# Kernel tuning notes

Hardware: AMD Instinct MI355X
Metric: run time of the kernel (lower is better)

Reference implementation:

```python
import jax, jax.numpy as jnp
import numpy as np

N_HEADS = 16

def setup_inputs() -> dict:
    key = jax.random.key(0)
    ks = jax.random.split(key, 6)
    B, S, D = 2, 2048, 1024
    sc = 0.02
    return {
        "x": jax.random.normal(ks[0], (B, S, D), dtype=jnp.float32),
        "Wq": jax.random.normal(ks[1], (D, D), dtype=jnp.float32) * sc,
        "Wk": jax.random.normal(ks[2], (D, D), dtype=jnp.float32) * sc,
        "Wv": jax.random.normal(ks[3], (D, D), dtype=jnp.float32) * sc,
        "Wo": jax.random.normal(ks[4], (D, D), dtype=jnp.float32) * sc,
        "bo": jnp.zeros((D,), dtype=jnp.float32),
        "stride": 64,
    }

def _strided_mask(S: int, stride: int):
    # local window |i-j|<=1  OR  |i-j| == k*stride (k>=1); diff==0 is in the window
    i = jnp.arange(S)[:, None]
    j = jnp.arange(S)[None, :]
    diff = jnp.abs(i - j)
    return (diff <= 1) | (diff % stride == 0)  # [S, S] bool

def reference(x, Wq, Wk, Wv, Wo, bo, stride):
    B, S, D = x.shape
    H = N_HEADS
    Dh = D // H
    # q/k/v projections: nn.Linear(bias=False) applies x @ W.T
    def proj(W):
        return (x @ W.T).reshape(B, S, H, Dh).transpose(0, 2, 1, 3)  # [B,H,S,Dh]
    q, k, v = proj(Wq), proj(Wk), proj(Wv)
    scores = jnp.einsum('bhqd,bhkd->bhqk', q, k) / jnp.sqrt(jnp.float32(Dh))
    mask = _strided_mask(S, stride)  # [S,S]
    scores = jnp.where(mask[None, None], scores, -jnp.inf)
    attn = jax.nn.softmax(scores, axis=-1)  # dropout is identity in eval
    out = jnp.einsum('bhqk,bhkd->bhqd', attn, v)  # [B,H,S,Dh]
    out = out.transpose(0, 2, 1, 3).reshape(B, S, D)
    return out @ Wo.T + bo
```

## Files before the change

kernel.cpp:

```cpp
#include <hip/hip_runtime.h>
#include <hip/hip_bf16.h>


typedef __bf16 bf16;
typedef __attribute__((ext_vector_type(4))) __bf16 bf16x4;
typedef __attribute__((ext_vector_type(8))) __bf16 bf16x8;
typedef __attribute__((ext_vector_type(4))) float f32x4;
typedef __attribute__((ext_vector_type(4))) unsigned int u32x4;

constexpr int S_ = 2048;
constexpr int D_ = 1024;
constexpr int H_ = 16;
constexpr int DH = 64;
constexpr int M_ = 2 * S_;

__device__ __forceinline__ void gload_lds16(const bf16* g, bf16* l) {
    __builtin_amdgcn_global_load_lds(
        (const __attribute__((address_space(1))) void*)g,
        (__attribute__((address_space(3))) void*)l, 16, 0, 0);
}

#define BARRIER_FULL() do { asm volatile("" ::: "memory"); \
    __builtin_amdgcn_sched_barrier(0); \
    __builtin_amdgcn_s_barrier(); \
    __builtin_amdgcn_sched_barrier(0); \
    asm volatile("" ::: "memory"); } while (0)

#define WAIT_VM0() do { asm volatile("s_waitcnt vmcnt(0)" ::: "memory"); \
    __builtin_amdgcn_sched_barrier(0); } while (0)

#define WAIT_VM4() do { asm volatile("s_waitcnt vmcnt(4)" ::: "memory"); \
    __builtin_amdgcn_sched_barrier(0); } while (0)

__device__ __forceinline__ void stage32(const bf16* __restrict__ G, int base_row,
                                        int kcol, bf16* lds, int wave, int lane)
{
    const int rIn = lane >> 2;
    const int g   = (lane & 3) ^ ((lane >> 2) & 3) ^ (lane >> 4);
    #pragma unroll
    for (int l = 0; l < 2; ++l) {
        const int R = (wave * 2 + l) * 16;
        gload_lds16(G + (size_t)(base_row + R + rIn) * D_ + kcol + g * 8,
                    lds + R * 32);
    }
}

__global__ __launch_bounds__(512, 2)
void gemm_qkv_p2(const bf16* __restrict__ A,
                 const bf16* __restrict__ W,
                 bf16* __restrict__ C)
{
    constexpr int BK = 32;
    constexpr int NT = D_ / BK;
    constexpr int TSLOT = 256 * BK;
    __shared__ __align__(16) bf16 As[3 * TSLOT];
    __shared__ __align__(16) bf16 Bs[3 * TSLOT];

    const int tid  = threadIdx.x;
    const int wave = tid >> 6;
    const int lane = tid & 63;
    const int wm = wave >> 2;
    const int wn = wave & 3;

    const int lid = blockIdx.y * 12 + blockIdx.x;
    const int xcd = lid & 7, pos = lid >> 3;
    const int bxs = (xcd & 1) * 6 + pos % 6;
    const int bys = (xcd >> 1) * 4 + pos / 6;
    const int bm = bys * 256;
    const int bn = bxs * 256;

    const int l15 = lane & 15;
    const int rs  = (lane >> 4) ^ (lane & 3) ^ ((lane >> 2) & 3);
    const int aRd = wm * 4096 + l15 * 32 + rs * 8;
    const int bRd = wn * 2048 + l15 * 32 + rs * 8;

    f32x4 acc[8][4];
    #pragma unroll
    for (int i = 0; i < 8; ++i)
        #pragma unroll
        for (int j = 0; j < 4; ++j) acc[i][j] = f32x4{0.f, 0.f, 0.f, 0.f};

    bf16x8 aF[4], bF[4];

    stage32(A, bm, 0,  As,         wave, lane);
    stage32(W, bn, 0,  Bs,         wave, lane);
    stage32(A, bm, BK, As + TSLOT, wave, lane);
    stage32(W, bn, BK, Bs + TSLOT, wave, lane);
    WAIT_VM4();
    BARRIER_FULL();

    int cur = 0;
    for (int t = 0; t < NT; ++t) {
        const int ss = (cur + 2 >= 3) ? (cur - 1) : (cur + 2);
        const bf16* aslot = As + cur * TSLOT;
        const bf16* bslot = Bs + cur * TSLOT;
        const bool pre = (t + 2) < NT;

        if (pre) {
            const int kn = (t + 2) * BK;
            stage32(A, bm, kn, As + ss * TSLOT, wave, lane);
            stage32(W, bn, kn, Bs + ss * TSLOT, wave, lane);
        }

        #pragma unroll
        for (int fn = 0; fn < 4; ++fn)
            bF[fn] = *(const bf16x8*)(bslot + bRd + fn * 512);
        #pragma unroll
        for (int fm = 0; fm < 4; ++fm)
            aF[fm] = *(const bf16x8*)(aslot + aRd + fm * 512);
        __builtin_amdgcn_s_setprio(1);
        #pragma unroll
        for (int fm = 0; fm < 4; ++fm)
            #pragma unroll
            for (int fn = 0; fn < 4; ++fn)
                acc[fm][fn] = __builtin_amdgcn_mfma_f32_16x16x32_bf16(
                    aF[fm], bF[fn], acc[fm][fn], 0, 0, 0);
        __builtin_amdgcn_s_setprio(0);
        #pragma unroll
        for (int fm = 0; fm < 4; ++fm)
            aF[fm] = *(const bf16x8*)(aslot + aRd + 2048 + fm * 512);
        __builtin_amdgcn_s_setprio(1);
        #pragma unroll
        for (int fm = 0; fm < 4; ++fm)
            #pragma unroll
            for (int fn = 0; fn < 4; ++fn)
                acc[4 + fm][fn] = __builtin_amdgcn_mfma_f32_16x16x32_bf16(
                    aF[fm], bF[fn], acc[4 + fm][fn], 0, 0, 0);
        __builtin_amdgcn_s_setprio(0);

        if (pre) { WAIT_VM4(); } else { WAIT_VM0(); }
        BARRIER_FULL();
        cur = (cur + 1 >= 3) ? 0 : (cur + 1);
    }

    #pragma unroll
    for (int fm8 = 0; fm8 < 8; ++fm8) {
        #pragma unroll
        for (int fn4 = 0; fn4 < 4; ++fn4) {
            const int n = bn + wn * 64 + fn4 * 16 + l15;
            const int z = n >> 10, col = n & 1023;
            bf16* Cz = C + (size_t)z * M_ * D_;
            const int mb = bm + wm * 128 + fm8 * 16 + (lane >> 4) * 4;
            #pragma unroll
            for (int r2 = 0; r2 < 4; ++r2)
                Cz[(size_t)(mb + r2) * D_ + col] = (bf16)acc[fm8][fn4][r2];
        }
    }
}

__global__ __launch_bounds__(256)
void gemm_o_p2(const bf16* __restrict__ A,
               const bf16* __restrict__ W,
               float* __restrict__ Cf,
               const float* __restrict__ bias)
{
    constexpr int BK = 32;
    constexpr int NT = D_ / BK;
    constexpr int TSLOT = 128 * BK;
    __shared__ __align__(16) bf16 As[3 * TSLOT];
    __shared__ __align__(16) bf16 Bs[3 * TSLOT];

    const int tid  = threadIdx.x;
    const int wave = tid >> 6;
    const int lane = tid & 63;
    const int wm = wave >> 1;
    const int wn = wave & 1;

    const int lid = blockIdx.y * 8 + blockIdx.x;
    const int xcd = lid & 7, pos = lid >> 3;
    const int bxs = (xcd & 3) * 2 + (pos & 1);
    const int bys = (xcd >> 2) * 16 + (pos >> 1);
    const int bm = bys * 128;
    const int bn = bxs * 128;

    const int l15 = lane & 15;
    const int rs  = (lane >> 4) ^ (lane & 3) ^ ((lane >> 2) & 3);
    const int aRd = wm * 2048 + l15 * 32 + rs * 8;
    const int bRd = wn * 2048 + l15 * 32 + rs * 8;

    f32x4 acc[4][4];
    #pragma unroll
    for (int i = 0; i < 4; ++i)
        #pragma unroll
        for (int j = 0; j < 4; ++j) acc[i][j] = f32x4{0.f, 0.f, 0.f, 0.f};

    bf16x8 aF[4], bF[4];

    stage32(A, bm, 0,  As,         wave, lane);
    stage32(W, bn, 0,  Bs,         wave, lane);
    stage32(A, bm, BK, As + TSLOT, wave, lane);
    stage32(W, bn, BK, Bs + TSLOT, wave, lane);
    WAIT_VM4();
    BARRIER_FULL();

    int cur = 0;
    for (int t = 0; t < NT; ++t) {
        const int ss = (cur + 2 >= 3) ? (cur - 1) : (cur + 2);
        const bf16* aslot = As + cur * TSLOT;
        const bf16* bslot = Bs + cur * TSLOT;
        const bool pre = (t + 2) < NT;

        if (pre) {
            const int kn = (t + 2) * BK;
            stage32(A, bm, kn, As + ss * TSLOT, wave, lane);
            stage32(W, bn, kn, Bs + ss * TSLOT, wave, lane);
        }
        #pragma unroll
        for (int fn = 0; fn < 4; ++fn)
            bF[fn] = *(const bf16x8*)(bslot + bRd + fn * 512);
        #pragma unroll
        for (int fm = 0; fm < 4; ++fm)
            aF[fm] = *(const bf16x8*)(aslot + aRd + fm * 512);
        __builtin_amdgcn_s_setprio(1);
        #pragma unroll
        for (int fm = 0; fm < 4; ++fm)
            #pragma unroll
            for (int fn = 0; fn < 4; ++fn)
                acc[fm][fn] = __builtin_amdgcn_mfma_f32_16x16x32_bf16(
                    aF[fm], bF[fn], acc[fm][fn], 0, 0, 0);
        __builtin_amdgcn_s_setprio(0);

        if (pre) { WAIT_VM4(); } else { WAIT_VM0(); }
        BARRIER_FULL();
        cur = (cur + 1 >= 3) ? 0 : (cur + 1);
    }

    #pragma unroll
    for (int fm = 0; fm < 4; ++fm) {
        #pragma unroll
        for (int fn = 0; fn < 4; ++fn) {
            const int n = bn + wn * 64 + fn * 16 + l15;
            const float bv = bias[n];
            const int mb = bm + wm * 64 + fm * 16 + (lane >> 4) * 4;
            #pragma unroll
            for (int r2 = 0; r2 < 4; ++r2)
                Cf[(size_t)(mb + r2) * D_ + n] = acc[fm][fn][r2] + bv;
        }
    }
}

template<bool AF32, bool BF32, bool CF32, bool BIAS>
__global__ __launch_bounds__(256)
void gemm_bt(const void* __restrict__ Av,
             const void* __restrict__ W0v, const void* __restrict__ W1v,
             const void* __restrict__ W2v,
             void* __restrict__ Cv, const float* __restrict__ bias)
{
    constexpr int BM = 128, BK = 64;
    constexpr int N = D_, K = D_;
    __shared__ __align__(16) bf16 As[BM * BK];
    __shared__ __align__(16) bf16 Bs[BM * BK];

    const int z = blockIdx.z;
    const void* Wv_ = (z == 0) ? W0v : (z == 1) ? W1v : W2v;

    const int tid  = threadIdx.x;
    const int wave = tid >> 6;
    const int lane = tid & 63;

    int bxs = blockIdx.x, bys = blockIdx.y;
    if (gridDim.z == 1 && gridDim.x == 8 && gridDim.y == 32) {
        const int lid = blockIdx.y * 8 + blockIdx.x;
        const int xcd = lid & 7, pos = lid >> 3;
        bxs = pos & 7;
        bys = xcd * 4 + (pos >> 3);
    }
    const int bm = bys * BM;
    const int bn = bxs * BM;
    const int wr = wave >> 1;
    const int wc = wave & 1;

    f32x4 acc[4][4];
    #pragma unroll
    for (int i = 0; i < 4; ++i)
        #pragma unroll
        for (int j = 0; j < 4; ++j)
            acc[i][j] = f32x4{0.f, 0.f, 0.f, 0.f};

    const int ldRow = lane >> 3;
    const int ldCol = (lane & 7) * 8;

    for (int kt = 0; kt < K; kt += BK) {
        if (AF32) {
            const float* A = (const float*)Av;
            #pragma unroll
            for (int it = 0; it < 8; ++it) {
                const int flat = (it * 256 + tid) * 4;
                const int row = flat >> 6, col = flat & 63;
                const float4 v = *(const float4*)(A + (size_t)(bm + row) * K + kt + col);
                bf16x4 p = { (bf16)v.x, (bf16)v.y, (bf16)v.z, (bf16)v.w };
                *(bf16x4*)&As[row * BK + col] = p;
            }
        } else {
            const bf16* A = (const bf16*)Av;
            #pragma unroll
            for (int q = 0; q < 4; ++q) {
                const int c = wave * 4 + q;
                const int row = c * 8 + ldRow;
                gload_lds16(A + (size_t)(bm + row) * K + kt + ldCol, &As[c * 8 * BK]);
            }
        }
        if (BF32) {
            const float* W = (const float*)Wv_;
            #pragma unroll
            for (int it = 0; it < 8; ++it) {
                const int flat = (it * 256 + tid) * 4;
                const int row = flat >> 6, col = flat & 63;
                const float4 v = *(const float4*)(W + (size_t)(bn + row) * K + kt + col);
                bf16x4 p = { (bf16)v.x, (bf16)v.y, (bf16)v.z, (bf16)v.w };
                *(bf16x4*)&Bs[row * BK + col] = p;
            }
        } else {
            const bf16* W = (const bf16*)Wv_;
            #pragma unroll
            for (int q = 0; q < 4; ++q) {
                const int c = wave * 4 + q;
                const int row = c * 8 + ldRow;
                gload_lds16(W + (size_t)(bn + row) * K + kt + ldCol, &Bs[c * 8 * BK]);
            }
        }
        __syncthreads();
        #pragma unroll
        for (int kk = 0; kk < 2; ++kk) {
            const int k0 = kk * 32 + (lane >> 4) * 8;
            bf16x8 af[4], bfv[4];
            #pragma unroll
            for (int mi = 0; mi < 4; ++mi)
                af[mi] = *(const bf16x8*)&As[(wr * 64 + mi * 16 + (lane & 15)) * BK + k0];
            #pragma unroll
            for (int ni = 0; ni < 4; ++ni)
                bfv[ni] = *(const bf16x8*)&Bs[(wc * 64 + ni * 16 + (lane & 15)) * BK + k0];
            #pragma unroll
            for (int mi = 0; mi < 4; ++mi)
                #pragma unroll
                for (int ni = 0; ni < 4; ++ni)
                    acc[mi][ni] = __builtin_amdgcn_mfma_f32_16x16x32_bf16(
                        af[mi], bfv[ni], acc[mi][ni], 0, 0, 0);
        }
        __syncthreads();
    }

    #pragma unroll
    for (int mi = 0; mi < 4; ++mi) {
        #pragma unroll
        for (int ni = 0; ni < 4; ++ni) {
            const int n  = bn + wc * 64 + ni * 16 + (lane & 15);
            const int mb = bm + wr * 64 + mi * 16 + (lane >> 4) * 4;
            float bv = 0.f;
            if (BIAS) bv = bias[n];
            #pragma unroll
            for (int r2 = 0; r2 < 4; ++r2) {
                const int m = mb + r2;
                if (CF32) {
                    ((float*)Cv)[(size_t)m * N + n] = acc[mi][ni][r2] + bv;
                } else {
                    bf16* Cc = (bf16*)Cv + (size_t)z * M_ * D_;
                    Cc[(size_t)m * N + n] = (bf16)(acc[mi][ni][r2] + bv);
                }
            }
        }
    }
}

__global__ __launch_bounds__(256)
void convert_to_bf16(const float* __restrict__ x,
                     const float* __restrict__ w0, const float* __restrict__ w1,
                     const float* __restrict__ w2, const float* __restrict__ w3,
                     bf16* __restrict__ out)
{
    const size_t eid = ((size_t)blockIdx.x * 256 + threadIdx.x) * 8;
    const float* src; size_t off;
    if (eid < (size_t)(1u << 22)) { src = x; off = eid; }
    else {
        const size_t t = eid - (1u << 22);
        const int k = (int)(t >> 20);
        off = t & ((1u << 20) - 1);
        src = (k == 0) ? w0 : (k == 1) ? w1 : (k == 2) ? w2 : w3;
    }
    const float4 a = *(const float4*)(src + off);
    const float4 c = *(const float4*)(src + off + 4);
    bf16x8 v = { (bf16)a.x, (bf16)a.y, (bf16)a.z, (bf16)a.w,
                 (bf16)c.x, (bf16)c.y, (bf16)c.z, (bf16)c.w };
    *(bf16x8*)(out + eid) = v;
}

__device__ __forceinline__ unsigned pk2bf(float lo, float hi) {
    const unsigned a = __builtin_bit_cast(unsigned short, (bf16)lo);
    const unsigned b = __builtin_bit_cast(unsigned short, (bf16)hi);
    return a | (b << 16);
}

__global__ __launch_bounds__(256)
void attn_mfma(bf16* __restrict__ QA, const bf16* __restrict__ Kw,
               const bf16* __restrict__ Vw)
{
    const int lane = threadIdx.x & 63;
    const int wid  = blockIdx.x * 4 + (threadIdx.x >> 6);
    const int r = wid & 63;
    const int h = (wid >> 6) & (H_ - 1);
    const int b = wid >> 10;

    const int qlo = lane & 15;
    const int g   = lane >> 4;
    const size_t rb = (size_t)b * S_;
    const int col0 = h * DH;
    const float scale = 0.125f;

    f32x4 accS[2][2];
    #pragma unroll
    for (int a = 0; a < 2; ++a)
        #pragma unroll
        for (int c = 0; c < 2; ++c) accS[a][c] = f32x4{0.f,0.f,0.f,0.f};

    #pragma unroll
    for (int c = 0; c < 2; ++c) {
        bf16x8 kf[2], qf[2];
        #pragma unroll
        for (int t = 0; t < 2; ++t) {
            const size_t row = rb + (size_t)(r + 64 * (t * 16 + qlo));
            kf[t] = *(const bf16x8*)&Kw[row * D_ + col0 + c * 32 + g * 8];
            qf[t] = *(const bf16x8*)&QA[row * D_ + col0 + c * 32 + g * 8];
        }
        #pragma unroll
        for (int kt = 0; kt < 2; ++kt)
            #pragma unroll
            for (int qt = 0; qt < 2; ++qt)
                accS[kt][qt] = __builtin_amdgcn_mfma_f32_16x16x32_bf16(
                    kf[kt], qf[qt], accS[kt][qt], 0, 0, 0);
    }

    const int s_nb = lane & 31;
    const int side = lane >> 5;
    const int i_nb = r + 64 * s_nb;
    const int j_nb = side ? (i_nb + 1) : (i_nb - 1);
    const bool nbv = (unsigned)j_nb < (unsigned)S_;
    const int j_sf = nbv ? j_nb : i_nb;
    float nbd = 0.f;
    #pragma unroll
    for (int t = 0; t < 8; ++t) {
        const bf16x8 qv = *(const bf16x8*)&QA[(rb + i_nb) * D_ + col0 + t * 8];
        const bf16x8 kv = *(const bf16x8*)&Kw[(rb + j_sf) * D_ + col0 + t * 8];
        #pragma unroll
        for (int e = 0; e < 8; ++e) nbd += (float)qv[e] * (float)kv[e];
    }
    const float NEGINF = -__builtin_inff();
    float nb = nbv ? nbd * scale : NEGINF;

    float mx[2] = { NEGINF, NEGINF };
    #pragma unroll
    for (int kt = 0; kt < 2; ++kt)
        #pragma unroll
        for (int qt = 0; qt < 2; ++qt)
            #pragma unroll
            for (int rr = 0; rr < 4; ++rr)
                mx[qt] = fmaxf(mx[qt], accS[kt][qt][rr]);
    mx[0] *= scale; mx[1] *= scale;
    mx[g & 1] = fmaxf(mx[g & 1], nb);
    #pragma unroll
    for (int x = 16; x <= 32; x <<= 1) {
        mx[0] = fmaxf(mx[0], __shfl_xor(mx[0], x));
        mx[1] = fmaxf(mx[1], __shfl_xor(mx[1], x));
    }
    float p[2][2][4];
    float sm[2] = { 0.f, 0.f };
    #pragma unroll
    for (int kt = 0; kt < 2; ++kt)
        #pragma unroll
        for (int qt = 0; qt < 2; ++qt)
            #pragma unroll
            for (int rr = 0; rr < 4; ++rr) {
                const float e = __expf(accS[kt][qt][rr] * scale - mx[qt]);
                p[kt][qt][rr] = e;
                sm[qt] += e;
            }
    float nbp = __expf(nb - mx[g & 1]);
    sm[g & 1] += nbp;
    #pragma unroll
    for (int x = 16; x <= 32; x <<= 1) {
        sm[0] += __shfl_xor(sm[0], x);
        sm[1] += __shfl_xor(sm[1], x);
    }
    const float inv[2] = { 1.f / sm[0], 1.f / sm[1] };
    #pragma unroll
    for (int kt = 0; kt < 2; ++kt)
        #pragma unroll
        for (int qt = 0; qt < 2; ++qt)
            #pragma unroll
            for (int rr = 0; rr < 4; ++rr) p[kt][qt][rr] *= inv[qt];
    nbp *= inv[g & 1];

    unsigned pk_[2][2][2];
    #pragma unroll
    for (int qt = 0; qt < 2; ++qt)
        #pragma unroll
        for (int kt = 0; kt < 2; ++kt)
            #pragma unroll
            for (int w = 0; w < 2; ++w)
                pk_[qt][kt][w] = pk2bf(p[kt][qt][2 * w], p[kt][qt][2 * w + 1]);

    const int srcA = qlo + 32 * (g & 1);
    const int srcB = srcA + 16;
    const int kts  = g >> 1;
    bf16x8 pa[2];
    #pragma unroll
    for (int qt = 0; qt < 2; ++qt) {
        u32x4 fr;
        #pragma unroll
        for (int w = 0; w < 2; ++w) {
            const unsigned a0 = (unsigned)__shfl((int)pk_[qt][0][w], srcA);
            const unsigned a1 = (unsigned)__shfl((int)pk_[qt][1][w], srcA);
            fr[w] = kts ? a1 : a0;
            const unsigned b0 = (unsigned)__shfl((int)pk_[qt][0][w], srcB);
            const unsigned b1 = (unsigned)__shfl((int)pk_[qt][1][w], srcB);
            fr[2 + w] = kts ? b1 : b0;
        }
        pa[qt] = __builtin_bit_cast(bf16x8, fr);
    }

    f32x4 accO[2][4];
    #pragma unroll
    for (int qt = 0; qt < 2; ++qt)
        #pragma unroll
        for (int dt = 0; dt < 4; ++dt) accO[qt][dt] = f32x4{0.f,0.f,0.f,0.f};
    #pragma unroll
    for (int dt = 0; dt < 4; ++dt) {
        bf16x8 vf;
        #pragma unroll
        for (int e = 0; e < 8; ++e)
            vf[e] = Vw[(rb + (size_t)(r + 64 * (g * 8 + e))) * D_ + col0 + dt * 16 + qlo];
        accO[0][dt] = __builtin_amdgcn_mfma_f32_16x16x32_bf16(pa[0], vf, accO[0][dt], 0, 0, 0);
        accO[1][dt] = __builtin_amdgcn_mfma_f32_16x16x32_bf16(pa[1], vf, accO[1][dt], 0, 0, 0);
    }

    #pragma unroll
    for (int qt = 0; qt < 2; ++qt)
        #pragma unroll
        for (int rr = 0; rr < 4; ++rr) {
            const int q  = qt * 16 + g * 4 + rr;
            const int iq = r + 64 * q;
            const float pm = __shfl(nbp, q);
            const float pp = __shfl(nbp, q + 32);
            const int jm = iq > 0 ? iq - 1 : 0;
            const int jp = iq < S_ - 1 ? iq + 1 : S_ - 1;
            #pragma unroll
            for (int dt = 0; dt < 4; ++dt) {
                const int d = col0 + dt * 16 + qlo;
                const float vm = (float)Vw[(rb + jm) * D_ + d];
                const float vp = (float)Vw[(rb + jp) * D_ + d];
                const float o = accO[qt][dt][rr] + pm * vm + pp * vp;
                QA[(rb + iq) * D_ + d] = (bf16)o;
            }
        }
}

extern "C" void kernel_launch(void* const* d_in, const int* in_sizes, int n_in,
                              void* d_out, int out_size, void* d_ws, size_t ws_size,
                              hipStream_t stream)
{
    const float* x  = (const float*)d_in[0];
    const float* Wq = (const float*)d_in[1];
    const float* Wk = (const float*)d_in[2];
    const float* Wv = (const float*)d_in[3];
    const float* Wo = (const float*)d_in[4];
    const float* bo = (const float*)d_in[5];

    bf16* qws = (bf16*)d_ws;
    bf16* kws = qws + (size_t)M_ * D_;
    bf16* vws = kws + (size_t)M_ * D_;

    const bool fast = ws_size >= (size_t)40 * 1024 * 1024;

    if (fast) {
        bf16* xb  = vws + (size_t)M_ * D_;
        bf16* wqb = xb + (1u << 22);
        bf16* wob = wqb + 3 * (1u << 20);

        convert_to_bf16<<<4096, 256, 0, stream>>>(x, Wq, Wk, Wv, Wo, xb);

        gemm_qkv_p2<<<dim3(3 * D_ / 256, M_ / 256), 512, 0, stream>>>(xb, wqb, qws);

        attn_mfma<<<dim3(2 * H_ * 64 / 4), 256, 0, stream>>>(qws, kws, vws);

        gemm_o_p2<<<dim3(D_ / 128, M_ / 128), 256, 0, stream>>>(
            qws, wob, (float*)d_out, bo);
    } else {
        gemm_bt<true, true, false, false><<<dim3(D_/128, M_/128, 3), 256, 0, stream>>>(
            x, Wq, Wk, Wv, qws, nullptr);

        attn_mfma<<<dim3(2 * H_ * 64 / 4), 256, 0, stream>>>(qws, kws, vws);

        gemm_bt<false, true, true, true><<<dim3(D_/128, M_/128, 1), 256, 0, stream>>>(
            qws, Wo, nullptr, nullptr, (float*)d_out, bo);
    }
}
```

Before: 103.1 us.

## Split GEMM k-steps into two barrier-separated phases with interleaved prefetch

Both the QKV and output-projection GEMM main loops now run in two phases per k-tile. Each phase reads LDS fragments, issues half of the next global-to-LDS prefetch, then waits on a barrier and lgkmcnt before its MFMAs. This is meant to spread memory issue across the compute and keep waves in lockstep. The output GEMM also moves to 512 threads with BK=64, a new XOR-swizzled stage64 layout and 4x2 per-wave tiles. Launch bounds drop to one block per CU, and the fallback gemm_bt no longer remaps its block order. The extra barriers add sync cost and the lower occupancy may hide less latency.

Result: faster. 87.07 us (-15.5%).

```diff
diff --git a/kernel.cpp b/kernel.cpp
--- a/kernel.cpp
+++ b/kernel.cpp
@@ -26,6 +26,9 @@
     __builtin_amdgcn_sched_barrier(0); \
     asm volatile("" ::: "memory"); } while (0)
 
+#define WAIT_LGKM0() do { asm volatile("s_waitcnt lgkmcnt(0)" ::: "memory"); \
+    __builtin_amdgcn_sched_barrier(0); } while (0)
+
 #define WAIT_VM0() do { asm volatile("s_waitcnt vmcnt(0)" ::: "memory"); \
     __builtin_amdgcn_sched_barrier(0); } while (0)
 
@@ -45,7 +48,7 @@
     }
 }
 
-__global__ __launch_bounds__(512, 2)
+__global__ __launch_bounds__(512, 1)
 void gemm_qkv_p2(const bf16* __restrict__ A,
                  const bf16* __restrict__ W,
                  bf16* __restrict__ C)
@@ -82,6 +85,23 @@
 
     bf16x8 aF[4], bF[4];
 
+#define READA_HALF(HH) do { _Pragma("unroll") \
+    for (int fm = 0; fm < 4; ++fm) \
+        aF[fm] = *(const bf16x8*)(aslot + aRd + (HH) * 2048 + fm * 512); \
+    } while (0)
+
+#define READB_ALL() do { _Pragma("unroll") \
+    for (int fn = 0; fn < 4; ++fn) \
+        bF[fn] = *(const bf16x8*)(bslot + bRd + fn * 512); \
+    } while (0)
+
+#define MFMA16(HH) do { _Pragma("unroll") \
+    for (int fm = 0; fm < 4; ++fm) { _Pragma("unroll") \
+        for (int fn = 0; fn < 4; ++fn) \
+            acc[(HH) * 4 + fm][fn] = __builtin_amdgcn_mfma_f32_16x16x32_bf16( \
+                aF[fm], bF[fn], acc[(HH) * 4 + fm][fn], 0, 0, 0); \
+    } } while (0)
+
     stage32(A, bm, 0,  As,         wave, lane);
     stage32(W, bn, 0,  Bs,         wave, lane);
     stage32(A, bm, BK, As + TSLOT, wave, lane);
@@ -95,43 +115,27 @@
         const bf16* aslot = As + cur * TSLOT;
         const bf16* bslot = Bs + cur * TSLOT;
         const bool pre = (t + 2) < NT;
-
-        if (pre) {
-            const int kn = (t + 2) * BK;
-            stage32(A, bm, kn, As + ss * TSLOT, wave, lane);
-            stage32(W, bn, kn, Bs + ss * TSLOT, wave, lane);
-        }
-
-        #pragma unroll
-        for (int fn = 0; fn < 4; ++fn)
-            bF[fn] = *(const bf16x8*)(bslot + bRd + fn * 512);
-        #pragma unroll
-        for (int fm = 0; fm < 4; ++fm)
-            aF[fm] = *(const bf16x8*)(aslot + aRd + fm * 512);
-        __builtin_amdgcn_s_setprio(1);
-        #pragma unroll
-        for (int fm = 0; fm < 4; ++fm)
-            #pragma unroll
-            for (int fn = 0; fn < 4; ++fn)
-                acc[fm][fn] = __builtin_amdgcn_mfma_f32_16x16x32_bf16(
-                    aF[fm], bF[fn], acc[fm][fn], 0, 0, 0);
-        __builtin_amdgcn_s_setprio(0);
-        #pragma unroll
-        for (int fm = 0; fm < 4; ++fm)
-            aF[fm] = *(const bf16x8*)(aslot + aRd + 2048 + fm * 512);
-        __builtin_amdgcn_s_setprio(1);
-        #pragma unroll
-        for (int fm = 0; fm < 4; ++fm)
-            #pragma unroll
-            for (int fn = 0; fn < 4; ++fn)
-                acc[4 + fm][fn] = __builtin_amdgcn_mfma_f32_16x16x32_bf16(
-                    aF[fm], bF[fn], acc[4 + fm][fn], 0, 0, 0);
-        __builtin_amdgcn_s_setprio(0);
-
+        const int kn = (t + 2) * BK;
+
+        READB_ALL();
+        READA_HALF(0);
+        if (pre) stage32(A, bm, kn, As + ss * TSLOT, wave, lane);
+        BARRIER_FULL(); WAIT_LGKM0();
+        __builtin_amdgcn_s_setprio(1); MFMA16(0); __builtin_amdgcn_s_setprio(0);
+        BARRIER_FULL();
+
+        READA_HALF(1);
+        if (pre) stage32(W, bn, kn, Bs + ss * TSLOT, wave, lane);
+        BARRIER_FULL(); WAIT_LGKM0();
+        __builtin_amdgcn_s_setprio(1); MFMA16(1); __builtin_amdgcn_s_setprio(0);
         if (pre) { WAIT_VM4(); } else { WAIT_VM0(); }
         BARRIER_FULL();
+
         cur = (cur + 1 >= 3) ? 0 : (cur + 1);
     }
+#undef READA_HALF
+#undef READB_ALL
+#undef MFMA16
 
     #pragma unroll
     for (int fm8 = 0; fm8 < 8; ++fm8) {
@@ -148,13 +152,26 @@
     }
 }
 
-__global__ __launch_bounds__(256)
-void gemm_o_p2(const bf16* __restrict__ A,
-               const bf16* __restrict__ W,
-               float* __restrict__ Cf,
-               const float* __restrict__ bias)
-{
-    constexpr int BK = 32;
+__device__ __forceinline__ void stage64(const bf16* __restrict__ G, int base_row,
+                                        int kcol, bf16* lds, int wave, int lane)
+{
+    const int rIn = lane >> 3;
+    const int g   = (lane & 7) ^ rIn;
+    #pragma unroll
+    for (int l = 0; l < 2; ++l) {
+        const int c = wave * 2 + l;
+        gload_lds16(G + (size_t)(base_row + c * 8 + rIn) * D_ + kcol + g * 8,
+                    lds + c * 512);
+    }
+}
+
+__global__ __launch_bounds__(512, 1)
+void gemm_o_2ph(const bf16* __restrict__ A,
+                const bf16* __restrict__ W,
+                float* __restrict__ Cf,
+                const float* __restrict__ bias)
+{
+    constexpr int BK = 64;
     constexpr int NT = D_ / BK;
     constexpr int TSLOT = 128 * BK;
     __shared__ __align__(16) bf16 As[3 * TSLOT];
@@ -163,8 +180,8 @@
     const int tid  = threadIdx.x;
     const int wave = tid >> 6;
     const int lane = tid & 63;
-    const int wm = wave >> 1;
-    const int wn = wave & 1;
+    const int wm = wave >> 2;
+    const int wn = wave & 3;
 
     const int lid = blockIdx.y * 8 + blockIdx.x;
     const int xcd = lid & 7, pos = lid >> 3;
@@ -174,22 +191,32 @@
     const int bn = bxs * 128;
 
     const int l15 = lane & 15;
-    const int rs  = (lane >> 4) ^ (lane & 3) ^ ((lane >> 2) & 3);
-    const int aRd = wm * 2048 + l15 * 32 + rs * 8;
-    const int bRd = wn * 2048 + l15 * 32 + rs * 8;
-
-    f32x4 acc[4][4];
+    const int hi  = lane >> 4;
+    const int r7  = l15 & 7;
+
+    int aOff[2][4], bOff[2][2];
+    #pragma unroll
+    for (int ks = 0; ks < 2; ++ks) {
+        #pragma unroll
+        for (int fm = 0; fm < 4; ++fm)
+            aOff[ks][fm] = (wm * 64 + fm * 16 + l15) * 64 + (((ks * 4 + hi) ^ r7) * 8);
+        #pragma unroll
+        for (int fn = 0; fn < 2; ++fn)
+            bOff[ks][fn] = (wn * 32 + fn * 16 + l15) * 64 + (((ks * 4 + hi) ^ r7) * 8);
+    }
+
+    f32x4 acc[4][2];
     #pragma unroll
     for (int i = 0; i < 4; ++i)
         #pragma unroll
-        for (int j = 0; j < 4; ++j) acc[i][j] = f32x4{0.f, 0.f, 0.f, 0.f};
-
-    bf16x8 aF[4], bF[4];
-
-    stage32(A, bm, 0,  As,         wave, lane);
-    stage32(W, bn, 0,  Bs,         wave, lane);
-    stage32(A, bm, BK, As + TSLOT, wave, lane);
-    stage32(W, bn, BK, Bs + TSLOT, wave, lane);
+        for (int j = 0; j < 2; ++j) acc[i][j] = f32x4{0.f, 0.f, 0.f, 0.f};
+
+    bf16x8 aF[4], bF[2][2];
+
+    stage64(A, bm, 0,  As,         wave, lane);
+    stage64(W, bn, 0,  Bs,         wave, lane);
+    stage64(A, bm, BK, As + TSLOT, wave, lane);
+    stage64(W, bn, BK, Bs + TSLOT, wave, lane);
     WAIT_VM4();
     BARRIER_FULL();
 
@@ -199,39 +226,54 @@
         const bf16* aslot = As + cur * TSLOT;
         const bf16* bslot = Bs + cur * TSLOT;
         const bool pre = (t + 2) < NT;
-
-        if (pre) {
-            const int kn = (t + 2) * BK;
-            stage32(A, bm, kn, As + ss * TSLOT, wave, lane);
-            stage32(W, bn, kn, Bs + ss * TSLOT, wave, lane);
-        }
-        #pragma unroll
-        for (int fn = 0; fn < 4; ++fn)
-            bF[fn] = *(const bf16x8*)(bslot + bRd + fn * 512);
+        const int kn = (t + 2) * BK;
+
+        #pragma unroll
+        for (int ks = 0; ks < 2; ++ks)
+            #pragma unroll
+            for (int fn = 0; fn < 2; ++fn)
+                bF[ks][fn] = *(const bf16x8*)(bslot + bOff[ks][fn]);
         #pragma unroll
         for (int fm = 0; fm < 4; ++fm)
-            aF[fm] = *(const bf16x8*)(aslot + aRd + fm * 512);
+            aF[fm] = *(const bf16x8*)(aslot + aOff[0][fm]);
+        if (pre) stage64(A, bm, kn, As + ss * TSLOT, wave, lane);
+        BARRIER_FULL(); WAIT_LGKM0();
         __builtin_amdgcn_s_setprio(1);
         #pragma unroll
         for (int fm = 0; fm < 4; ++fm)
             #pragma unroll
-            for (int fn = 0; fn < 4; ++fn)
+            for (int fn = 0; fn < 2; ++fn)
                 acc[fm][fn] = __builtin_amdgcn_mfma_f32_16x16x32_bf16(
-                    aF[fm], bF[fn], acc[fm][fn], 0, 0, 0);
+                    aF[fm], bF[0][fn], acc[fm][fn], 0, 0, 0);
         __builtin_amdgcn_s_setprio(0);
-
+        BARRIER_FULL();
+
+        #pragma unroll
+        for (int fm = 0; fm < 4; ++fm)
+            aF[fm] = *(const bf16x8*)(aslot + aOff[1][fm]);
+        if (pre) stage64(W, bn, kn, Bs + ss * TSLOT, wave, lane);
+        BARRIER_FULL(); WAIT_LGKM0();
+        __builtin_amdgcn_s_setprio(1);
+        #pragma unroll
+        for (int fm = 0; fm < 4; ++fm)
+            #pragma unroll
+            for (int fn = 0; fn < 2; ++fn)
+                acc[fm][fn] = __builtin_amdgcn_mfma_f32_16x16x32_bf16(
+                    aF[fm], bF[1][fn], acc[fm][fn], 0, 0, 0);
+        __builtin_amdgcn_s_setprio(0);
         if (pre) { WAIT_VM4(); } else { WAIT_VM0(); }
         BARRIER_FULL();
+
         cur = (cur + 1 >= 3) ? 0 : (cur + 1);
     }
 
     #pragma unroll
     for (int fm = 0; fm < 4; ++fm) {
         #pragma unroll
-        for (int fn = 0; fn < 4; ++fn) {
-            const int n = bn + wn * 64 + fn * 16 + l15;
+        for (int fn = 0; fn < 2; ++fn) {
+            const int n = bn + wn * 32 + fn * 16 + l15;
             const float bv = bias[n];
-            const int mb = bm + wm * 64 + fm * 16 + (lane >> 4) * 4;
+            const int mb = bm + wm * 64 + fm * 16 + hi * 4;
             #pragma unroll
             for (int r2 = 0; r2 < 4; ++r2)
                 Cf[(size_t)(mb + r2) * D_ + n] = acc[fm][fn][r2] + bv;
@@ -258,15 +300,8 @@
     const int wave = tid >> 6;
     const int lane = tid & 63;
 
-    int bxs = blockIdx.x, bys = blockIdx.y;
-    if (gridDim.z == 1 && gridDim.x == 8 && gridDim.y == 32) {
-        const int lid = blockIdx.y * 8 + blockIdx.x;
-        const int xcd = lid & 7, pos = lid >> 3;
-        bxs = pos & 7;
-        bys = xcd * 4 + (pos >> 3);
-    }
-    const int bm = bys * BM;
-    const int bn = bxs * BM;
+    const int bm = blockIdx.y * BM;
+    const int bn = blockIdx.x * BM;
     const int wr = wave >> 1;
     const int wc = wave & 1;
 
@@ -581,7 +616,7 @@
 
         attn_mfma<<<dim3(2 * H_ * 64 / 4), 256, 0, stream>>>(qws, kws, vws);
 
-        gemm_o_p2<<<dim3(D_ / 128, M_ / 128), 256, 0, stream>>>(
+        gemm_o_2ph<<<dim3(D_ / 128, M_ / 128), 512, 0, stream>>>(
             qws, wob, (float*)d_out, bo);
     } else {
         gemm_bt<true, true, false, false><<<dim3(D_/128, M_/128, 3), 256, 0, stream>>>(
```
